# Optimization experiments

Measured on AMD Instinct MI355X. Metric: run time of the kernel, lower is better.

Reference implementation:

```python
import jax, jax.numpy as jnp
import numpy as np

DIM = 2048
NUM_HEADS = 16
HEAD_DIM = 128
MAX_SEQ_LEN = 2048
ATTN_SCALE = 0.12
EPS = 1e-6


def _rms_norm(x):
    # RMSNorm without learned weight, over last dim
    return x * jax.lax.rsqrt(jnp.mean(jnp.square(x), axis=-1, keepdims=True) + EPS)


def _rope_tables(T):
    # half of the head dim rotates, half is identity (zero frequency)
    quarter = HEAD_DIM // 4
    angular_freq = (1.0 / 1024.0) ** jnp.linspace(0.0, 1.0, quarter, dtype=jnp.float32)
    angular_freq = jnp.concatenate([angular_freq, jnp.zeros(quarter, dtype=jnp.float32)])  # [D/2]
    t = jnp.arange(T, dtype=jnp.float32)
    theta = t[:, None] * angular_freq[None, :]  # [T, D/2]
    return jnp.cos(theta), jnp.sin(theta)


def _apply_rope(x, cos, sin):
    # x: [B, T, H, D]; cos/sin: [T, D/2] -> broadcast [1, T, 1, D/2]
    x1, x2 = jnp.split(x, 2, axis=-1)
    c = cos[None, :, None, :]
    s = sin[None, :, None, :]
    y1 = x1 * c + x2 * s
    y2 = -x1 * s + x2 * c
    return jnp.concatenate([y1, y2], axis=-1)


def setup_inputs() -> dict:
    key = jax.random.key(0)
    k1, k2, k3, k4 = jax.random.split(key, 4)
    hdim = NUM_HEADS * HEAD_DIM
    x = jax.random.normal(k1, (1, MAX_SEQ_LEN, DIM), dtype=jnp.float32)
    qkvo_w = jax.random.normal(k2, (4, hdim, DIM), dtype=jnp.float32) * (DIM ** -0.5)
    ve = jax.random.normal(k3, (1, MAX_SEQ_LEN, hdim), dtype=jnp.float32)
    lambdas = jax.random.uniform(k4, (2,), dtype=jnp.float32)
    return {"x": x, "qkvo_w": qkvo_w, "ve": ve, "lambdas": lambdas}


def reference(x, qkvo_w, ve, lambdas):
    B, T, _ = x.shape
    H, D = NUM_HEADS, HEAD_DIM
    # fused qkv projection: [B, T, 3*H*D]
    qkv = jnp.einsum('btc,ehc->bteh', x, qkvo_w[:3]).reshape(B, T, 3, H, D)
    q, k, v = qkv[:, :, 0], qkv[:, :, 1], qkv[:, :, 2]  # each [B, T, H, D]
    q, k, v = _rms_norm(q), _rms_norm(k), _rms_norm(v)
    cos, sin = _rope_tables(T)
    q = _apply_rope(q, cos, sin)
    k = _apply_rope(k, cos, sin)
    v = lambdas[0] * v + lambdas[1] * ve.reshape(B, T, H, D)
    # causal attention with fixed scale
    scores = jnp.einsum('bthd,bshd->bhts', q, k) * ATTN_SCALE  # [B, H, T, T]
    causal = jnp.tril(jnp.ones((T, T), dtype=bool))
    scores = jnp.where(causal[None, None], scores, -jnp.inf)
    p = jax.nn.softmax(scores, axis=-1)
    y = jnp.einsum('bhts,bshd->bthd', p, v).reshape(B, T, H * D)
    return jnp.einsum('bth,ch->btc', y, qkvo_w[3])
```

## Files before the change

kernel.cpp:

```cpp
#include <hip/hip_runtime.h>
#include <math.h>

#define SEQ  2048
#define CDIM 2048
#define NH   16
#define DH   128
#define HDIM 2048

typedef __attribute__((ext_vector_type(8))) short  bf16x8;
typedef __attribute__((ext_vector_type(4))) float  f32x4;
typedef unsigned short ushort_t;

__device__ __forceinline__ unsigned short f2bf(float f) {
  unsigned u = __float_as_uint(f);
  u = (u + 0x7fffu + ((u >> 16) & 1u)) >> 16;
  return (unsigned short)u;
}
__device__ __forceinline__ float b2f(unsigned short s) {
  return __uint_as_float((unsigned)s << 16);
}

__device__ __forceinline__ void async_ld16(const ushort_t* g, ushort_t* l) {
  __builtin_amdgcn_global_load_lds((const __attribute__((address_space(1))) unsigned int*)g,
                                   (__attribute__((address_space(3))) unsigned int*)l,
                                   16, 0, 0);
}

__device__ __forceinline__ f32x4 mfma16(bf16x8 a, bf16x8 b, f32x4 c) {
  return __builtin_amdgcn_mfma_f32_16x16x32_bf16(a, b, c, 0, 0, 0);
}

__global__ __launch_bounds__(256) void to_bf16(const float* __restrict__ src,
                                               ushort_t* __restrict__ dst, int n8) {
  int i = blockIdx.x * 256 + threadIdx.x;
  if (i >= n8) return;
  const float4* s = (const float4*)src;
  float4 f0 = s[i * 2], f1 = s[i * 2 + 1];
  bf16x8 o;
  o[0] = (short)f2bf(f0.x); o[1] = (short)f2bf(f0.y);
  o[2] = (short)f2bf(f0.z); o[3] = (short)f2bf(f0.w);
  o[4] = (short)f2bf(f1.x); o[5] = (short)f2bf(f1.y);
  o[6] = (short)f2bf(f1.z); o[7] = (short)f2bf(f1.w);
  *(bf16x8*)&dst[i * 8] = o;
}

template <int OUT_BF16>
__global__ __launch_bounds__(256) void gemm_bf16(const ushort_t* __restrict__ A,
                                                 const ushort_t* __restrict__ B,
                                                 void* __restrict__ Cv,
                                                 long bStride, long cStride) {
  constexpr int K = CDIM, N = HDIM;
  __shared__ __align__(16) ushort_t As[128 * 32];
  __shared__ __align__(16) ushort_t Bs[128 * 32];
  const ushort_t* Bp = B + (long)blockIdx.z * bStride;
  const int m0 = blockIdx.y * 128, n0 = blockIdx.x * 128;
  const int tid = threadIdx.x, lane = tid & 63, wave = tid >> 6;
  const int wm = wave >> 1, wn = wave & 1;
  const int g = lane >> 4, l15 = lane & 15;
  const int srow = tid >> 2, scc = tid & 3;

  f32x4 acc[4][4];
#pragma unroll
  for (int i = 0; i < 4; ++i)
#pragma unroll
    for (int j = 0; j < 4; ++j) acc[i][j] = (f32x4)0.0f;

  for (int k0 = 0; k0 < K; k0 += 32) {
    __syncthreads();
    {
      int r0 = srow, r1 = srow + 64;
      int c0 = scc ^ ((r0 >> 1) & 3), c1 = scc ^ ((r1 >> 1) & 3);
      async_ld16(&A [(long)(m0 + r0) * K + k0 + c0 * 8], &As[wave * 512]);
      async_ld16(&A [(long)(m0 + r1) * K + k0 + c1 * 8], &As[2048 + wave * 512]);
      async_ld16(&Bp[(long)(n0 + r0) * K + k0 + c0 * 8], &Bs[wave * 512]);
      async_ld16(&Bp[(long)(n0 + r1) * K + k0 + c1 * 8], &Bs[2048 + wave * 512]);
    }
    __syncthreads();

    bf16x8 af[4], bfr[4];
#pragma unroll
    for (int mi = 0; mi < 4; ++mi) {
      int row = wm * 64 + mi * 16 + l15;
      int cc = g ^ ((row >> 1) & 3);
      af[mi] = *(const bf16x8*)&As[row * 32 + cc * 8];
    }
#pragma unroll
    for (int ni = 0; ni < 4; ++ni) {
      int row = wn * 64 + ni * 16 + l15;
      int cc = g ^ ((row >> 1) & 3);
      bfr[ni] = *(const bf16x8*)&Bs[row * 32 + cc * 8];
    }
#pragma unroll
    for (int mi = 0; mi < 4; ++mi)
#pragma unroll
      for (int ni = 0; ni < 4; ++ni)
        acc[mi][ni] = mfma16(af[mi], bfr[ni], acc[mi][ni]);
  }

#pragma unroll
  for (int mi = 0; mi < 4; ++mi)
#pragma unroll
    for (int ni = 0; ni < 4; ++ni) {
      int row = m0 + wm * 64 + mi * 16 + g * 4;
      int col = n0 + wn * 64 + ni * 16 + l15;
#pragma unroll
      for (int r = 0; r < 4; ++r) {
        if (OUT_BF16)
          ((ushort_t*)Cv)[cStride * blockIdx.z + (long)(row + r) * N + col] = f2bf(acc[mi][ni][r]);
        else
          ((float*)Cv)[(long)(row + r) * N + col] = acc[mi][ni][r];
      }
    }
}

__device__ __forceinline__ float wave_sum64(float x) {
#pragma unroll
  for (int m = 32; m >= 1; m >>= 1) x += __shfl_xor(x, m, 64);
  return x;
}

__global__ __launch_bounds__(64) void norm_rope(ushort_t* __restrict__ qkvb,
                                                const float* __restrict__ ve,
                                                const float* __restrict__ lambdas) {
  const int t = blockIdx.x, h = blockIdx.y, d = threadIdx.x;
  const long base = (long)t * HDIM + h * DH;
  ushort_t* q = qkvb + base;
  ushort_t* k = qkvb + (long)SEQ * HDIM + base;
  ushort_t* v = qkvb + 2L * SEQ * HDIM + base;

  float q1 = b2f(q[d]), q2 = b2f(q[d + 64]);
  float k1 = b2f(k[d]), k2 = b2f(k[d + 64]);
  float v1 = b2f(v[d]), v2 = b2f(v[d + 64]);

  float qsc = rsqrtf(wave_sum64(q1 * q1 + q2 * q2) * (1.0f / 128.0f) + 1e-6f);
  float ksc = rsqrtf(wave_sum64(k1 * k1 + k2 * k2) * (1.0f / 128.0f) + 1e-6f);
  float vsc = rsqrtf(wave_sum64(v1 * v1 + v2 * v2) * (1.0f / 128.0f) + 1e-6f);
  q1 *= qsc; q2 *= qsc;
  k1 *= ksc; k2 *= ksc;
  v1 *= vsc; v2 *= vsc;

  float freq = (d < 32) ? powf(1.0f / 1024.0f, (float)d * (1.0f / 31.0f)) : 0.0f;
  float th = (float)t * freq;
  float c = cosf(th), s = sinf(th);

  float qo1 = q1 * c + q2 * s, qo2 = -q1 * s + q2 * c;
  float ko1 = k1 * c + k2 * s, ko2 = -k1 * s + k2 * c;

  float l0 = lambdas[0], l1 = lambdas[1];
  const float* vep = ve + base;
  float vo1 = l0 * v1 + l1 * vep[d];
  float vo2 = l0 * v2 + l1 * vep[d + 64];

  q[d] = f2bf(qo1); q[d + 64] = f2bf(qo2);
  k[d] = f2bf(ko1); k[d + 64] = f2bf(ko2);
  v[d] = f2bf(vo1); v[d + 64] = f2bf(vo2);
}

__global__ __launch_bounds__(256) void transpose_v(const ushort_t* __restrict__ vb,
                                                   ushort_t* __restrict__ vbT) {
  __shared__ __align__(16) ushort_t L[64 * 136];
  const int t0 = blockIdx.x * 64, h = blockIdx.y;
  const int tid = threadIdx.x;
#pragma unroll
  for (int p = 0; p < 4; ++p) {
    int idx = p * 256 + tid;
    int row = idx >> 4, cc = idx & 15;
    *(bf16x8*)&L[row * 136 + cc * 8] =
        *(const bf16x8*)&vb[(long)(t0 + row) * HDIM + h * DH + cc * 8];
  }
  __syncthreads();
#pragma unroll
  for (int p = 0; p < 4; ++p) {
    int idx = p * 256 + tid;
    int d = idx >> 3, tc = (idx & 7) * 8;
    bf16x8 o;
#pragma unroll
    for (int j = 0; j < 8; ++j) o[j] = (short)L[(tc + j) * 136 + d];
    *(bf16x8*)&vbT[((long)h * DH + d) * SEQ + t0 + tc] = o;
  }
}

__global__ __launch_bounds__(128) void flash_mfma(const ushort_t* __restrict__ qkvb,
                                                  const ushort_t* __restrict__ vbT,
                                                  ushort_t* __restrict__ yb) {
  __shared__ __align__(16) ushort_t Ks[64 * 128];
  __shared__ __align__(16) ushort_t Vt[128 * 64];
  __shared__ __align__(16) ushort_t Ps[64 * 72];
  const int q0 = blockIdx.x * 64, h = blockIdx.y;
  const int tid = threadIdx.x, lane = tid & 63, wave = tid >> 6;
  const int g = lane >> 4, l15 = lane & 15;
  const ushort_t* Kg = qkvb + (long)SEQ * HDIM;
  const ushort_t* Vg = vbT + (long)h * DH * SEQ;

  bf16x8 qf[2][4];
#pragma unroll
  for (int nt = 0; nt < 2; ++nt)
#pragma unroll
    for (int ks = 0; ks < 4; ++ks)
      qf[nt][ks] = *(const bf16x8*)
          &qkvb[(long)(q0 + wave * 32 + nt * 16 + l15) * HDIM + h * DH + ks * 32 + g * 8];

  f32x4 oacc[2][8];
#pragma unroll
  for (int qt = 0; qt < 2; ++qt)
#pragma unroll
    for (int dt = 0; dt < 8; ++dt) oacc[qt][dt] = (f32x4)0.0f;
  float mrow[2] = {-1e30f, -1e30f}, lrow[2] = {0.0f, 0.0f};

  for (int s0 = 0; s0 <= q0; s0 += 64) {
    __syncthreads();
#pragma unroll
    for (int i = 0; i < 8; ++i) {
      int idx = i * 128 + tid;
      { int row = idx >> 4, cc = idx & 15, cg = cc ^ (row & 7);
        async_ld16(&Kg[(long)(s0 + row) * HDIM + h * DH + cg * 8], &Ks[i * 1024 + wave * 512]); }
      { int row = idx >> 3, cc = idx & 7,  cg = cc ^ (row & 7);
        async_ld16(&Vg[(long)row * SEQ + s0 + cg * 8], &Vt[i * 1024 + wave * 512]); }
    }
    __syncthreads();

    f32x4 st[2][4];
#pragma unroll
    for (int nt = 0; nt < 2; ++nt)
#pragma unroll
      for (int mt = 0; mt < 4; ++mt) st[nt][mt] = (f32x4)0.0f;
#pragma unroll
    for (int ks = 0; ks < 4; ++ks)
#pragma unroll
      for (int mt = 0; mt < 4; ++mt) {
        int row = mt * 16 + l15;
        int cg = ks * 4 + g;
        int cc = cg ^ (row & 7);
        bf16x8 a = *(const bf16x8*)&Ks[row * 128 + cc * 8];
        st[0][mt] = mfma16(a, qf[0][ks], st[0][mt]);
        st[1][mt] = mfma16(a, qf[1][ks], st[1][mt]);
      }

    float alpha_q[2];
#pragma unroll
    for (int nt = 0; nt < 2; ++nt) {
      const int qg = q0 + wave * 32 + nt * 16 + l15;
      float p[4][4];
      float tmax = -1e30f;
#pragma unroll
      for (int mt = 0; mt < 4; ++mt)
#pragma unroll
        for (int r = 0; r < 4; ++r) {
          float sv = st[nt][mt][r] * 0.12f;
          if (s0 + mt * 16 + g * 4 + r > qg) sv = -1e30f;
          p[mt][r] = sv;
          tmax = fmaxf(tmax, sv);
        }
      tmax = fmaxf(tmax, __shfl_xor(tmax, 16, 64));
      tmax = fmaxf(tmax, __shfl_xor(tmax, 32, 64));
      float nm = fmaxf(mrow[nt], tmax);
      float alpha = __expf(mrow[nt] - nm);
      float psum = 0.0f;
#pragma unroll
      for (int mt = 0; mt < 4; ++mt) {
        float e0 = __expf(p[mt][0] - nm), e1 = __expf(p[mt][1] - nm);
        float e2 = __expf(p[mt][2] - nm), e3 = __expf(p[mt][3] - nm);
        unsigned short b0 = f2bf(e0), b1 = f2bf(e1), b2 = f2bf(e2), b3 = f2bf(e3);
        psum += b2f(b0) + b2f(b1) + b2f(b2) + b2f(b3);
        unsigned lo = (unsigned)b0 | ((unsigned)b1 << 16);
        unsigned hi = (unsigned)b2 | ((unsigned)b3 << 16);
        *(uint2*)&Ps[(wave * 32 + nt * 16 + l15) * 72 + mt * 16 + g * 4] = make_uint2(lo, hi);
      }
      psum += __shfl_xor(psum, 16, 64);
      psum += __shfl_xor(psum, 32, 64);
      mrow[nt] = nm;
      lrow[nt] = lrow[nt] * alpha + psum;
      alpha_q[nt] = alpha;
    }

    float aO[2][4];
#pragma unroll
    for (int qt = 0; qt < 2; ++qt)
#pragma unroll
      for (int r = 0; r < 4; ++r)
        aO[qt][r] = __shfl(alpha_q[qt], g * 4 + r, 64);
#pragma unroll
    for (int qt = 0; qt < 2; ++qt)
#pragma unroll
      for (int dt = 0; dt < 8; ++dt)
#pragma unroll
        for (int r = 0; r < 4; ++r)
          oacc[qt][dt][r] *= aO[qt][r];

#pragma unroll
    for (int ks = 0; ks < 2; ++ks) {
      bf16x8 ap0 = *(const bf16x8*)&Ps[(wave * 32 + l15) * 72 + ks * 32 + g * 8];
      bf16x8 ap1 = *(const bf16x8*)&Ps[(wave * 32 + 16 + l15) * 72 + ks * 32 + g * 8];
#pragma unroll
      for (int dt = 0; dt < 8; ++dt) {
        int row = dt * 16 + l15;
        int cg = ks * 4 + g;
        int cc = cg ^ (row & 7);
        bf16x8 bv = *(const bf16x8*)&Vt[row * 64 + cc * 8];
        oacc[0][dt] = mfma16(ap0, bv, oacc[0][dt]);
        oacc[1][dt] = mfma16(ap1, bv, oacc[1][dt]);
      }
    }
  }

  float linv[2][4];
#pragma unroll
  for (int qt = 0; qt < 2; ++qt)
#pragma unroll
    for (int r = 0; r < 4; ++r)
      linv[qt][r] = 1.0f / __shfl(lrow[qt], g * 4 + r, 64);
#pragma unroll
  for (int qt = 0; qt < 2; ++qt)
#pragma unroll
    for (int dt = 0; dt < 8; ++dt) {
      int row = q0 + wave * 32 + qt * 16 + g * 4;
      int col = h * DH + dt * 16 + l15;
#pragma unroll
      for (int r = 0; r < 4; ++r)
        yb[(long)(row + r) * HDIM + col] = f2bf(oacc[qt][dt][r] * linv[qt][r]);
    }
}

extern "C" void kernel_launch(void* const* d_in, const int* in_sizes, int n_in,
                              void* d_out, int out_size, void* d_ws, size_t ws_size,
                              hipStream_t stream) {
  const float* x       = (const float*)d_in[0];
  const float* w       = (const float*)d_in[1];
  const float* ve      = (const float*)d_in[2];
  const float* lambdas = (const float*)d_in[3];
  float* out = (float*)d_out;

  char* ws = (char*)d_ws;
  ushort_t* qkvb = (ushort_t*)ws;
  ushort_t* xb   = (ushort_t*)(ws + 25165824);
  ushort_t* wb   = (ushort_t*)(ws + 33554432);
  ushort_t* vbT  = (ushort_t*)(ws + 67108864);
  ushort_t* yb   = xb;

  to_bf16<<<2048, 256, 0, stream>>>(x, xb, (SEQ * CDIM) / 8);
  to_bf16<<<8192, 256, 0, stream>>>(w, wb, (4 * HDIM * CDIM) / 8);
  gemm_bf16<1><<<dim3(16, 16, 3), 256, 0, stream>>>(xb, wb, qkvb,
                                                    (long)HDIM * CDIM, (long)SEQ * HDIM);
  norm_rope<<<dim3(SEQ, NH), 64, 0, stream>>>(qkvb, ve, lambdas);
  transpose_v<<<dim3(SEQ / 64, NH), 256, 0, stream>>>(qkvb + 2L * SEQ * HDIM, vbT);
  flash_mfma<<<dim3(SEQ / 64, NH), 128, 0, stream>>>(qkvb, vbT, yb);
  gemm_bf16<0><<<dim3(16, 16, 1), 256, 0, stream>>>(yb, wb + 3L * HDIM * CDIM, out, 0, 0);
}
```

Measured before the change: 341.3 us.

## Double-buffer K/V tiles and use four 16-row waves in flash attention

Restructures the flash attention kernel so 256 threads (four waves) each own 16 query rows instead of two waves owning 32. K and V tiles are now double-buffered in LDS, and the async loads for the next tile are issued before computing on the current one, to overlap global-load latency with MFMA work. Causal masking is applied only on the diagonal tile. Trade-offs: LDS use roughly doubles, which may cut occupancy, and correctness depends on the async LDS loads having completed before the barrier.

```diff
diff --git a/kernel.cpp b/kernel.cpp
--- a/kernel.cpp
+++ b/kernel.cpp
@@ -180,11 +180,11 @@
   }
 }
 
-__global__ __launch_bounds__(128) void flash_mfma(const ushort_t* __restrict__ qkvb,
+__global__ __launch_bounds__(256) void flash_mfma(const ushort_t* __restrict__ qkvb,
                                                   const ushort_t* __restrict__ vbT,
                                                   ushort_t* __restrict__ yb) {
-  __shared__ __align__(16) ushort_t Ks[64 * 128];
-  __shared__ __align__(16) ushort_t Vt[128 * 64];
+  __shared__ __align__(16) ushort_t Ks[2][64 * 128];
+  __shared__ __align__(16) ushort_t Vt[2][128 * 64];
   __shared__ __align__(16) ushort_t Ps[64 * 72];
   const int q0 = blockIdx.x * 64, h = blockIdx.y;
   const int tid = threadIdx.x, lane = tid & 63, wave = tid >> 6;
@@ -192,133 +192,120 @@
   const ushort_t* Kg = qkvb + (long)SEQ * HDIM;
   const ushort_t* Vg = vbT + (long)h * DH * SEQ;
 
-  bf16x8 qf[2][4];
-#pragma unroll
-  for (int nt = 0; nt < 2; ++nt)
-#pragma unroll
-    for (int ks = 0; ks < 4; ++ks)
-      qf[nt][ks] = *(const bf16x8*)
-          &qkvb[(long)(q0 + wave * 32 + nt * 16 + l15) * HDIM + h * DH + ks * 32 + g * 8];
-
-  f32x4 oacc[2][8];
-#pragma unroll
-  for (int qt = 0; qt < 2; ++qt)
-#pragma unroll
-    for (int dt = 0; dt < 8; ++dt) oacc[qt][dt] = (f32x4)0.0f;
-  float mrow[2] = {-1e30f, -1e30f}, lrow[2] = {0.0f, 0.0f};
-
+  bf16x8 qf[4];
+#pragma unroll
+  for (int ks = 0; ks < 4; ++ks)
+    qf[ks] = *(const bf16x8*)
+        &qkvb[(long)(q0 + wave * 16 + l15) * HDIM + h * DH + ks * 32 + g * 8];
+
+  f32x4 oacc[8];
+#pragma unroll
+  for (int dt = 0; dt < 8; ++dt) oacc[dt] = (f32x4)0.0f;
+  float mrow = -1e30f, lrow = 0.0f;
+
+  auto stage = [&](int buf, int s0) {
+#pragma unroll
+    for (int i = 0; i < 4; ++i) {
+      int idx = i * 256 + tid;
+      { int row = idx >> 4, cc = idx & 15, cg = cc ^ (row & 7);
+        async_ld16(&Kg[(long)(s0 + row) * HDIM + h * DH + cg * 8],
+                   &Ks[buf][i * 2048 + wave * 512]); }
+      { int row = idx >> 3, cc = idx & 7,  cg = cc ^ (row & 7);
+        async_ld16(&Vg[(long)row * SEQ + s0 + cg * 8],
+                   &Vt[buf][i * 2048 + wave * 512]); }
+    }
+  };
+
+  stage(0, 0);
+  int cur = 0;
   for (int s0 = 0; s0 <= q0; s0 += 64) {
     __syncthreads();
-#pragma unroll
-    for (int i = 0; i < 8; ++i) {
-      int idx = i * 128 + tid;
-      { int row = idx >> 4, cc = idx & 15, cg = cc ^ (row & 7);
-        async_ld16(&Kg[(long)(s0 + row) * HDIM + h * DH + cg * 8], &Ks[i * 1024 + wave * 512]); }
-      { int row = idx >> 3, cc = idx & 7,  cg = cc ^ (row & 7);
-        async_ld16(&Vg[(long)row * SEQ + s0 + cg * 8], &Vt[i * 1024 + wave * 512]); }
-    }
-    __syncthreads();
-
-    f32x4 st[2][4];
-#pragma unroll
-    for (int nt = 0; nt < 2; ++nt)
-#pragma unroll
-      for (int mt = 0; mt < 4; ++mt) st[nt][mt] = (f32x4)0.0f;
+    if (s0 + 64 <= q0) stage(cur ^ 1, s0 + 64);
+
+    f32x4 st[4];
+#pragma unroll
+    for (int mt = 0; mt < 4; ++mt) st[mt] = (f32x4)0.0f;
 #pragma unroll
     for (int ks = 0; ks < 4; ++ks)
 #pragma unroll
       for (int mt = 0; mt < 4; ++mt) {
         int row = mt * 16 + l15;
-        int cg = ks * 4 + g;
-        int cc = cg ^ (row & 7);
-        bf16x8 a = *(const bf16x8*)&Ks[row * 128 + cc * 8];
-        st[0][mt] = mfma16(a, qf[0][ks], st[0][mt]);
-        st[1][mt] = mfma16(a, qf[1][ks], st[1][mt]);
+        int cc = (ks * 4 + g) ^ (row & 7);
+        bf16x8 a = *(const bf16x8*)&Ks[cur][row * 128 + cc * 8];
+        st[mt] = mfma16(a, qf[ks], st[mt]);
       }
 
-    float alpha_q[2];
-#pragma unroll
-    for (int nt = 0; nt < 2; ++nt) {
-      const int qg = q0 + wave * 32 + nt * 16 + l15;
-      float p[4][4];
-      float tmax = -1e30f;
+    const int qg = q0 + wave * 16 + l15;
+    float p[4][4];
+#pragma unroll
+    for (int mt = 0; mt < 4; ++mt)
+#pragma unroll
+      for (int r = 0; r < 4; ++r) p[mt][r] = st[mt][r] * 0.12f;
+    if (s0 == q0) {
 #pragma unroll
       for (int mt = 0; mt < 4; ++mt)
 #pragma unroll
-        for (int r = 0; r < 4; ++r) {
-          float sv = st[nt][mt][r] * 0.12f;
-          if (s0 + mt * 16 + g * 4 + r > qg) sv = -1e30f;
-          p[mt][r] = sv;
-          tmax = fmaxf(tmax, sv);
-        }
-      tmax = fmaxf(tmax, __shfl_xor(tmax, 16, 64));
-      tmax = fmaxf(tmax, __shfl_xor(tmax, 32, 64));
-      float nm = fmaxf(mrow[nt], tmax);
-      float alpha = __expf(mrow[nt] - nm);
-      float psum = 0.0f;
-#pragma unroll
-      for (int mt = 0; mt < 4; ++mt) {
-        float e0 = __expf(p[mt][0] - nm), e1 = __expf(p[mt][1] - nm);
-        float e2 = __expf(p[mt][2] - nm), e3 = __expf(p[mt][3] - nm);
-        unsigned short b0 = f2bf(e0), b1 = f2bf(e1), b2 = f2bf(e2), b3 = f2bf(e3);
-        psum += b2f(b0) + b2f(b1) + b2f(b2) + b2f(b3);
-        unsigned lo = (unsigned)b0 | ((unsigned)b1 << 16);
-        unsigned hi = (unsigned)b2 | ((unsigned)b3 << 16);
-        *(uint2*)&Ps[(wave * 32 + nt * 16 + l15) * 72 + mt * 16 + g * 4] = make_uint2(lo, hi);
-      }
-      psum += __shfl_xor(psum, 16, 64);
-      psum += __shfl_xor(psum, 32, 64);
-      mrow[nt] = nm;
-      lrow[nt] = lrow[nt] * alpha + psum;
-      alpha_q[nt] = alpha;
-    }
-
-    float aO[2][4];
-#pragma unroll
-    for (int qt = 0; qt < 2; ++qt)
-#pragma unroll
-      for (int r = 0; r < 4; ++r)
-        aO[qt][r] = __shfl(alpha_q[qt], g * 4 + r, 64);
-#pragma unroll
-    for (int qt = 0; qt < 2; ++qt)
-#pragma unroll
-      for (int dt = 0; dt < 8; ++dt)
-#pragma unroll
         for (int r = 0; r < 4; ++r)
-          oacc[qt][dt][r] *= aO[qt][r];
+          if (s0 + mt * 16 + g * 4 + r > qg) p[mt][r] = -1e30f;
+    }
+    float tmax = -1e30f;
+#pragma unroll
+    for (int mt = 0; mt < 4; ++mt)
+#pragma unroll
+      for (int r = 0; r < 4; ++r) tmax = fmaxf(tmax, p[mt][r]);
+    tmax = fmaxf(tmax, __shfl_xor(tmax, 16, 64));
+    tmax = fmaxf(tmax, __shfl_xor(tmax, 32, 64));
+    float nm = fmaxf(mrow, tmax);
+    float alpha = __expf(mrow - nm);
+    float psum = 0.0f;
+#pragma unroll
+    for (int mt = 0; mt < 4; ++mt) {
+      float e0 = __expf(p[mt][0] - nm), e1 = __expf(p[mt][1] - nm);
+      float e2 = __expf(p[mt][2] - nm), e3 = __expf(p[mt][3] - nm);
+      unsigned short b0 = f2bf(e0), b1 = f2bf(e1), b2 = f2bf(e2), b3 = f2bf(e3);
+      psum += b2f(b0) + b2f(b1) + b2f(b2) + b2f(b3);
+      unsigned lo = (unsigned)b0 | ((unsigned)b1 << 16);
+      unsigned hi = (unsigned)b2 | ((unsigned)b3 << 16);
+      *(uint2*)&Ps[(wave * 16 + l15) * 72 + mt * 16 + g * 4] = make_uint2(lo, hi);
+    }
+    psum += __shfl_xor(psum, 16, 64);
+    psum += __shfl_xor(psum, 32, 64);
+    mrow = nm;
+    lrow = lrow * alpha + psum;
+
+    float aO[4];
+#pragma unroll
+    for (int r = 0; r < 4; ++r) aO[r] = __shfl(alpha, g * 4 + r, 64);
+#pragma unroll
+    for (int dt = 0; dt < 8; ++dt)
+#pragma unroll
+      for (int r = 0; r < 4; ++r) oacc[dt][r] *= aO[r];
 
 #pragma unroll
     for (int ks = 0; ks < 2; ++ks) {
-      bf16x8 ap0 = *(const bf16x8*)&Ps[(wave * 32 + l15) * 72 + ks * 32 + g * 8];
-      bf16x8 ap1 = *(const bf16x8*)&Ps[(wave * 32 + 16 + l15) * 72 + ks * 32 + g * 8];
+      bf16x8 ap = *(const bf16x8*)&Ps[(wave * 16 + l15) * 72 + ks * 32 + g * 8];
 #pragma unroll
       for (int dt = 0; dt < 8; ++dt) {
         int row = dt * 16 + l15;
-        int cg = ks * 4 + g;
-        int cc = cg ^ (row & 7);
-        bf16x8 bv = *(const bf16x8*)&Vt[row * 64 + cc * 8];
-        oacc[0][dt] = mfma16(ap0, bv, oacc[0][dt]);
-        oacc[1][dt] = mfma16(ap1, bv, oacc[1][dt]);
+        int cc = (ks * 4 + g) ^ (row & 7);
+        bf16x8 bv = *(const bf16x8*)&Vt[cur][row * 64 + cc * 8];
+        oacc[dt] = mfma16(ap, bv, oacc[dt]);
       }
     }
-  }
-
-  float linv[2][4];
-#pragma unroll
-  for (int qt = 0; qt < 2; ++qt)
+    cur ^= 1;
+  }
+
+  float linv[4];
+#pragma unroll
+  for (int r = 0; r < 4; ++r) linv[r] = 1.0f / __shfl(lrow, g * 4 + r, 64);
+#pragma unroll
+  for (int dt = 0; dt < 8; ++dt) {
+    int row = q0 + wave * 16 + g * 4;
+    int col = h * DH + dt * 16 + l15;
 #pragma unroll
     for (int r = 0; r < 4; ++r)
-      linv[qt][r] = 1.0f / __shfl(lrow[qt], g * 4 + r, 64);
-#pragma unroll
-  for (int qt = 0; qt < 2; ++qt)
-#pragma unroll
-    for (int dt = 0; dt < 8; ++dt) {
-      int row = q0 + wave * 32 + qt * 16 + g * 4;
-      int col = h * DH + dt * 16 + l15;
-#pragma unroll
-      for (int r = 0; r < 4; ++r)
-        yb[(long)(row + r) * HDIM + col] = f2bf(oacc[qt][dt][r] * linv[qt][r]);
-    }
+      yb[(long)(row + r) * HDIM + col] = f2bf(oacc[dt][r] * linv[r]);
+  }
 }
 
 extern "C" void kernel_launch(void* const* d_in, const int* in_sizes, int n_in,
@@ -343,6 +330,6 @@
                                                     (long)HDIM * CDIM, (long)SEQ * HDIM);
   norm_rope<<<dim3(SEQ, NH), 64, 0, stream>>>(qkvb, ve, lambdas);
   transpose_v<<<dim3(SEQ / 64, NH), 256, 0, stream>>>(qkvb + 2L * SEQ * HDIM, vbT);
-  flash_mfma<<<dim3(SEQ / 64, NH), 128, 0, stream>>>(qkvb, vbT, yb);
+  flash_mfma<<<dim3(SEQ / 64, NH), 256, 0, stream>>>(qkvb, vbT, yb);
   gemm_bf16<0><<<dim3(16, 16, 1), 256, 0, stream>>>(yb, wb + 3L * HDIM * CDIM, out, 0, 0);
 }
```

Result: faster. 319.8 us (-6.3%).

## Split KV range across wave pairs in flash attention with pipelined K staging

Applied to the files above, without the earlier changes.

The flash attention kernel goes from 128 to 256 threads. Two wave pairs each take alternate 64-key tiles for the same 64 query rows, and their partial softmax states are merged through shared memory at the end. K tiles are prefetched asynchronously into a 4-slot ring buffer. V fragments are now read straight from global memory instead of being staged in LDS. The change also reverses block order for half the heads to balance causal load, skips masking on non-diagonal tiles, swizzles the P buffer, and raises wave priority around MFMA sections. Together these aim to cut per-block serial latency and barrier stalls, at the cost of more global V traffic and an extra merge step.

```diff
diff --git a/kernel.cpp b/kernel.cpp
--- a/kernel.cpp
+++ b/kernel.cpp
@@ -180,14 +180,16 @@
   }
 }
 
-__global__ __launch_bounds__(128) void flash_mfma(const ushort_t* __restrict__ qkvb,
-                                                  const ushort_t* __restrict__ vbT,
-                                                  ushort_t* __restrict__ yb) {
-  __shared__ __align__(16) ushort_t Ks[64 * 128];
-  __shared__ __align__(16) ushort_t Vt[128 * 64];
-  __shared__ __align__(16) ushort_t Ps[64 * 72];
-  const int q0 = blockIdx.x * 64, h = blockIdx.y;
+__global__ __launch_bounds__(256, 2) void flash_mfma(const ushort_t* __restrict__ qkvb,
+                                                     const ushort_t* __restrict__ vbT,
+                                                     ushort_t* __restrict__ yb) {
+  __shared__ __align__(16) ushort_t Ks[4 * 64 * 128];
+  __shared__ __align__(16) ushort_t Ps[4 * 32 * 64];
+  const int h = blockIdx.y;
+  const int qi = (h < 8) ? blockIdx.x : (31 - blockIdx.x);
+  const int q0 = qi * 64;
   const int tid = threadIdx.x, lane = tid & 63, wave = tid >> 6;
+  const int pair = wave >> 1, qhalf = wave & 1;
   const int g = lane >> 4, l15 = lane & 15;
   const ushort_t* Kg = qkvb + (long)SEQ * HDIM;
   const ushort_t* Vg = vbT + (long)h * DH * SEQ;
@@ -198,127 +200,185 @@
 #pragma unroll
     for (int ks = 0; ks < 4; ++ks)
       qf[nt][ks] = *(const bf16x8*)
-          &qkvb[(long)(q0 + wave * 32 + nt * 16 + l15) * HDIM + h * DH + ks * 32 + g * 8];
+          &qkvb[(long)(q0 + qhalf * 32 + nt * 16 + l15) * HDIM + h * DH + ks * 32 + g * 8];
 
   f32x4 oacc[2][8];
 #pragma unroll
-  for (int qt = 0; qt < 2; ++qt)
-#pragma unroll
-    for (int dt = 0; dt < 8; ++dt) oacc[qt][dt] = (f32x4)0.0f;
+  for (int nt = 0; nt < 2; ++nt)
+#pragma unroll
+    for (int dt = 0; dt < 8; ++dt) oacc[nt][dt] = (f32x4)0.0f;
   float mrow[2] = {-1e30f, -1e30f}, lrow[2] = {0.0f, 0.0f};
 
-  for (int s0 = 0; s0 <= q0; s0 += 64) {
+  auto stage = [&](int t) {
+    ushort_t* dst = &Ks[(t & 3) * 8192];
+#pragma unroll
+    for (int i = 0; i < 4; ++i) {
+      int idx = i * 256 + tid;
+      int row = idx >> 4, cc = idx & 15, cg = cc ^ (row & 7);
+      async_ld16(&Kg[(long)(t * 64 + row) * HDIM + h * DH + cg * 8],
+                 dst + i * 2048 + wave * 512);
+    }
+  };
+
+  stage(0);
+  if (qi >= 1) stage(1);
+  const int J = (qi + 2) >> 1;
+
+  for (int j = 0; j < J; ++j) {
     __syncthreads();
-#pragma unroll
-    for (int i = 0; i < 8; ++i) {
-      int idx = i * 128 + tid;
-      { int row = idx >> 4, cc = idx & 15, cg = cc ^ (row & 7);
-        async_ld16(&Kg[(long)(s0 + row) * HDIM + h * DH + cg * 8], &Ks[i * 1024 + wave * 512]); }
-      { int row = idx >> 3, cc = idx & 7,  cg = cc ^ (row & 7);
-        async_ld16(&Vg[(long)row * SEQ + s0 + cg * 8], &Vt[i * 1024 + wave * 512]); }
-    }
-    __syncthreads();
-
-    f32x4 st[2][4];
-#pragma unroll
-    for (int nt = 0; nt < 2; ++nt)
-#pragma unroll
-      for (int mt = 0; mt < 4; ++mt) st[nt][mt] = (f32x4)0.0f;
-#pragma unroll
-    for (int ks = 0; ks < 4; ++ks)
-#pragma unroll
-      for (int mt = 0; mt < 4; ++mt) {
-        int row = mt * 16 + l15;
-        int cg = ks * 4 + g;
-        int cc = cg ^ (row & 7);
-        bf16x8 a = *(const bf16x8*)&Ks[row * 128 + cc * 8];
-        st[0][mt] = mfma16(a, qf[0][ks], st[0][mt]);
-        st[1][mt] = mfma16(a, qf[1][ks], st[1][mt]);
-      }
-
-    float alpha_q[2];
+    {
+      int t2 = 2 * j + 2;
+      if (t2 <= qi)     stage(t2);
+      if (t2 + 1 <= qi) stage(t2 + 1);
+    }
+    const int tt = 2 * j + pair;
+    if (tt <= qi) {
+      const ushort_t* Kb = &Ks[(tt & 3) * 8192];
+
+      f32x4 st[2][4];
+#pragma unroll
+      for (int nt = 0; nt < 2; ++nt)
+#pragma unroll
+        for (int mt = 0; mt < 4; ++mt) st[nt][mt] = (f32x4)0.0f;
+      __builtin_amdgcn_s_setprio(1);
+#pragma unroll
+      for (int ks = 0; ks < 4; ++ks)
+#pragma unroll
+        for (int mt = 0; mt < 4; ++mt) {
+          int row = mt * 16 + l15;
+          int cc = (ks * 4 + g) ^ (row & 7);
+          bf16x8 a = *(const bf16x8*)&Kb[row * 128 + cc * 8];
+          st[0][mt] = mfma16(a, qf[0][ks], st[0][mt]);
+          st[1][mt] = mfma16(a, qf[1][ks], st[1][mt]);
+        }
+      __builtin_amdgcn_s_setprio(0);
+
+      float alpha_nt[2];
+#pragma unroll
+      for (int nt = 0; nt < 2; ++nt) {
+        const int qg = q0 + qhalf * 32 + nt * 16 + l15;
+        float p[4][4];
+#pragma unroll
+        for (int mt = 0; mt < 4; ++mt)
+#pragma unroll
+          for (int r = 0; r < 4; ++r) p[mt][r] = st[nt][mt][r] * 0.12f;
+        if (tt == qi) {
+#pragma unroll
+          for (int mt = 0; mt < 4; ++mt)
+#pragma unroll
+            for (int r = 0; r < 4; ++r)
+              if (tt * 64 + mt * 16 + g * 4 + r > qg) p[mt][r] = -1e30f;
+        }
+        float tmax = -1e30f;
+#pragma unroll
+        for (int mt = 0; mt < 4; ++mt)
+#pragma unroll
+          for (int r = 0; r < 4; ++r) tmax = fmaxf(tmax, p[mt][r]);
+        tmax = fmaxf(tmax, __shfl_xor(tmax, 16, 64));
+        tmax = fmaxf(tmax, __shfl_xor(tmax, 32, 64));
+        float nm = fmaxf(mrow[nt], tmax);
+        float alpha = __expf(mrow[nt] - nm);
+        float psum = 0.0f;
+        const int prow = nt * 16 + l15;
+        char* pbase = (char*)&Ps[wave * 2048] + prow * 128;
+#pragma unroll
+        for (int mt = 0; mt < 4; ++mt) {
+          float e0 = __expf(p[mt][0] - nm), e1 = __expf(p[mt][1] - nm);
+          float e2 = __expf(p[mt][2] - nm), e3 = __expf(p[mt][3] - nm);
+          unsigned short b0 = f2bf(e0), b1 = f2bf(e1), b2 = f2bf(e2), b3 = f2bf(e3);
+          psum += b2f(b0) + b2f(b1) + b2f(b2) + b2f(b3);
+          unsigned lo = (unsigned)b0 | ((unsigned)b1 << 16);
+          unsigned hi = (unsigned)b2 | ((unsigned)b3 << 16);
+          int byt = (mt * 32 + g * 8) ^ ((prow & 7) << 4);
+          *(uint2*)(pbase + byt) = make_uint2(lo, hi);
+        }
+        psum += __shfl_xor(psum, 16, 64);
+        psum += __shfl_xor(psum, 32, 64);
+        mrow[nt] = nm;
+        lrow[nt] = lrow[nt] * alpha + psum;
+        alpha_nt[nt] = alpha;
+      }
+
+#pragma unroll
+      for (int nt = 0; nt < 2; ++nt) {
+        float aO[4];
+#pragma unroll
+        for (int r = 0; r < 4; ++r) aO[r] = __shfl(alpha_nt[nt], g * 4 + r, 64);
+#pragma unroll
+        for (int dt = 0; dt < 8; ++dt)
+#pragma unroll
+          for (int r = 0; r < 4; ++r) oacc[nt][dt][r] *= aO[r];
+      }
+
+      bf16x8 ap[2][2];
+#pragma unroll
+      for (int nt = 0; nt < 2; ++nt)
+#pragma unroll
+        for (int ks = 0; ks < 2; ++ks) {
+          const int prow = nt * 16 + l15;
+          int byt = (ks * 64 + g * 16) ^ ((prow & 7) << 4);
+          ap[nt][ks] = *(const bf16x8*)((char*)&Ps[wave * 2048] + prow * 128 + byt);
+        }
+      __builtin_amdgcn_s_setprio(1);
+#pragma unroll
+      for (int dt = 0; dt < 8; ++dt) {
+        bf16x8 bv0 = *(const bf16x8*)&Vg[(long)(dt * 16 + l15) * SEQ + tt * 64 + g * 8];
+        bf16x8 bv1 = *(const bf16x8*)&Vg[(long)(dt * 16 + l15) * SEQ + tt * 64 + 32 + g * 8];
+        oacc[0][dt] = mfma16(ap[0][0], bv0, oacc[0][dt]);
+        oacc[0][dt] = mfma16(ap[0][1], bv1, oacc[0][dt]);
+        oacc[1][dt] = mfma16(ap[1][0], bv0, oacc[1][dt]);
+        oacc[1][dt] = mfma16(ap[1][1], bv1, oacc[1][dt]);
+      }
+      __builtin_amdgcn_s_setprio(0);
+    }
+  }
+
+  __syncthreads();
+  float* Xo = (float*)Ks;
+  float* ML = (float*)Ps;
+  if (pair == 1) {
+    float* dst = Xo + qhalf * 4096;
 #pragma unroll
     for (int nt = 0; nt < 2; ++nt) {
-      const int qg = q0 + wave * 32 + nt * 16 + l15;
-      float p[4][4];
-      float tmax = -1e30f;
-#pragma unroll
-      for (int mt = 0; mt < 4; ++mt)
+#pragma unroll
+      for (int dt = 0; dt < 8; ++dt)
+        *(f32x4*)&dst[(nt * 8 + dt) * 256 + lane * 4] = oacc[nt][dt];
+      if (g == 0) {
+        ML[((qhalf * 2 + nt) * 16 + l15) * 2 + 0] = mrow[nt];
+        ML[((qhalf * 2 + nt) * 16 + l15) * 2 + 1] = lrow[nt];
+      }
+    }
+  }
+  __syncthreads();
+  if (pair == 0) {
+    const float* src = Xo + qhalf * 4096;
+#pragma unroll
+    for (int nt = 0; nt < 2; ++nt) {
+      float m2 = ML[((qhalf * 2 + nt) * 16 + l15) * 2 + 0];
+      float l2 = ML[((qhalf * 2 + nt) * 16 + l15) * 2 + 1];
+      float M  = fmaxf(mrow[nt], m2);
+      float a0 = __expf(mrow[nt] - M), a2 = __expf(m2 - M);
+      float li = 1.0f / (a0 * lrow[nt] + a2 * l2);
+      float a0r[4], a2r[4], lir[4];
+#pragma unroll
+      for (int r = 0; r < 4; ++r) {
+        a0r[r] = __shfl(a0, g * 4 + r, 64);
+        a2r[r] = __shfl(a2, g * 4 + r, 64);
+        lir[r] = __shfl(li, g * 4 + r, 64);
+      }
+#pragma unroll
+      for (int dt = 0; dt < 8; ++dt) {
+        f32x4 o2 = *(const f32x4*)&src[(nt * 8 + dt) * 256 + lane * 4];
+        int row = q0 + qhalf * 32 + nt * 16 + g * 4;
+        int col = h * DH + dt * 16 + l15;
 #pragma unroll
         for (int r = 0; r < 4; ++r) {
-          float sv = st[nt][mt][r] * 0.12f;
-          if (s0 + mt * 16 + g * 4 + r > qg) sv = -1e30f;
-          p[mt][r] = sv;
-          tmax = fmaxf(tmax, sv);
+          float v = (a0r[r] * oacc[nt][dt][r] + a2r[r] * o2[r]) * lir[r];
+          yb[(long)(row + r) * HDIM + col] = f2bf(v);
         }
-      tmax = fmaxf(tmax, __shfl_xor(tmax, 16, 64));
-      tmax = fmaxf(tmax, __shfl_xor(tmax, 32, 64));
-      float nm = fmaxf(mrow[nt], tmax);
-      float alpha = __expf(mrow[nt] - nm);
-      float psum = 0.0f;
-#pragma unroll
-      for (int mt = 0; mt < 4; ++mt) {
-        float e0 = __expf(p[mt][0] - nm), e1 = __expf(p[mt][1] - nm);
-        float e2 = __expf(p[mt][2] - nm), e3 = __expf(p[mt][3] - nm);
-        unsigned short b0 = f2bf(e0), b1 = f2bf(e1), b2 = f2bf(e2), b3 = f2bf(e3);
-        psum += b2f(b0) + b2f(b1) + b2f(b2) + b2f(b3);
-        unsigned lo = (unsigned)b0 | ((unsigned)b1 << 16);
-        unsigned hi = (unsigned)b2 | ((unsigned)b3 << 16);
-        *(uint2*)&Ps[(wave * 32 + nt * 16 + l15) * 72 + mt * 16 + g * 4] = make_uint2(lo, hi);
-      }
-      psum += __shfl_xor(psum, 16, 64);
-      psum += __shfl_xor(psum, 32, 64);
-      mrow[nt] = nm;
-      lrow[nt] = lrow[nt] * alpha + psum;
-      alpha_q[nt] = alpha;
-    }
-
-    float aO[2][4];
-#pragma unroll
-    for (int qt = 0; qt < 2; ++qt)
-#pragma unroll
-      for (int r = 0; r < 4; ++r)
-        aO[qt][r] = __shfl(alpha_q[qt], g * 4 + r, 64);
-#pragma unroll
-    for (int qt = 0; qt < 2; ++qt)
-#pragma unroll
-      for (int dt = 0; dt < 8; ++dt)
-#pragma unroll
-        for (int r = 0; r < 4; ++r)
-          oacc[qt][dt][r] *= aO[qt][r];
-
-#pragma unroll
-    for (int ks = 0; ks < 2; ++ks) {
-      bf16x8 ap0 = *(const bf16x8*)&Ps[(wave * 32 + l15) * 72 + ks * 32 + g * 8];
-      bf16x8 ap1 = *(const bf16x8*)&Ps[(wave * 32 + 16 + l15) * 72 + ks * 32 + g * 8];
-#pragma unroll
-      for (int dt = 0; dt < 8; ++dt) {
-        int row = dt * 16 + l15;
-        int cg = ks * 4 + g;
-        int cc = cg ^ (row & 7);
-        bf16x8 bv = *(const bf16x8*)&Vt[row * 64 + cc * 8];
-        oacc[0][dt] = mfma16(ap0, bv, oacc[0][dt]);
-        oacc[1][dt] = mfma16(ap1, bv, oacc[1][dt]);
-      }
-    }
-  }
-
-  float linv[2][4];
-#pragma unroll
-  for (int qt = 0; qt < 2; ++qt)
-#pragma unroll
-    for (int r = 0; r < 4; ++r)
-      linv[qt][r] = 1.0f / __shfl(lrow[qt], g * 4 + r, 64);
-#pragma unroll
-  for (int qt = 0; qt < 2; ++qt)
-#pragma unroll
-    for (int dt = 0; dt < 8; ++dt) {
-      int row = q0 + wave * 32 + qt * 16 + g * 4;
-      int col = h * DH + dt * 16 + l15;
-#pragma unroll
-      for (int r = 0; r < 4; ++r)
-        yb[(long)(row + r) * HDIM + col] = f2bf(oacc[qt][dt][r] * linv[qt][r]);
-    }
+      }
+    }
+  }
 }
 
 extern "C" void kernel_launch(void* const* d_in, const int* in_sizes, int n_in,
@@ -343,6 +403,6 @@
                                                     (long)HDIM * CDIM, (long)SEQ * HDIM);
   norm_rope<<<dim3(SEQ, NH), 64, 0, stream>>>(qkvb, ve, lambdas);
   transpose_v<<<dim3(SEQ / 64, NH), 256, 0, stream>>>(qkvb + 2L * SEQ * HDIM, vbT);
-  flash_mfma<<<dim3(SEQ / 64, NH), 128, 0, stream>>>(qkvb, vbT, yb);
+  flash_mfma<<<dim3(SEQ / 64, NH), 256, 0, stream>>>(qkvb, vbT, yb);
   gemm_bf16<0><<<dim3(16, 16, 1), 256, 0, stream>>>(yb, wb + 3L * HDIM * CDIM, out, 0, 0);
 }
```

New measurement: 317.9 us. -6.8%, faster.
